# Kernel tuning notes

Hardware: AMD Instinct MI355X
Metric: run time of the kernel (lower is better)

Reference implementation:

```python
import jax, jax.numpy as jnp
import numpy as np

KSIZE = 3
PAD = (KSIZE - 1) // 2
SIG = 0.3 * ((KSIZE - 1) * 0.5 - 1) + 0.8  # sigma_space == sigma_density == 0.8
INV2S2 = 1.0 / (2.0 * SIG * SIG)


def _gauss_space():
    c = KSIZE // 2
    xs = np.arange(KSIZE, dtype=np.float32)
    gx, gy = np.meshgrid(xs, xs, indexing='xy')
    w = np.exp(-(((gx - c) ** 2 + (gy - c) ** 2)) * INV2S2)
    w = w / w.sum()
    return jnp.asarray(w, dtype=jnp.float32)


def _patches(x):
    # x: [N,C,H,W] -> [N,C,H,W,k,k], zero padding (matches F.pad value=0)
    H, W = x.shape[-2], x.shape[-1]
    xp = jnp.pad(x, ((0, 0), (0, 0), (PAD, PAD), (PAD, PAD)))
    rows = []
    for i in range(KSIZE):
        cols = [xp[:, :, i:i + H, j:j + W] for j in range(KSIZE)]
        rows.append(jnp.stack(cols, axis=-1))
    return jnp.stack(rows, axis=-2)


def setup_inputs() -> dict:
    key = jax.random.key(0)
    k1, k2, k3 = jax.random.split(key, 3)
    B, V, C, H, W = 2, 4, 3, 512, 512
    depth = jax.random.uniform(k1, (B, V, 1, H, W), dtype=jnp.float32)
    color = jax.random.uniform(k2, (B, V, C, H, W), dtype=jnp.float32)
    mask = jax.random.uniform(k3, (B, V, 1, H, W), dtype=jnp.float32)
    return {"depth": depth, "color": color, "mask": mask}


def reference(depth, color, mask):
    B, V, C, H, W = color.shape
    d = depth.reshape(B * V, 1, H, W)
    m = mask.reshape(B * V, 1, H, W)
    c = color.reshape(B * V, C, H, W)

    dp = _patches(d)  # [N,1,H,W,k,k]
    cp = _patches(c)  # [N,C,H,W,k,k]
    mp = _patches(m)  # [N,1,H,W,k,k]

    # depth (density) gaussian weight, normalized per-pixel over the window
    wd = jnp.exp(-((dp - d[..., None, None]) ** 2) * INV2S2)
    wd = wd / wd.sum(axis=(-1, -2), keepdims=True)

    # color gaussian weight summed over channels, normalized per-pixel
    wc = jnp.exp(-((cp - c[..., None, None]) ** 2) * INV2S2).sum(axis=1, keepdims=True)
    wc = wc / wc.sum(axis=(-1, -2), keepdims=True)

    ws = _gauss_space().reshape(1, 1, 1, 1, KSIZE, KSIZE)

    w = wd * wc * ws * mp + 1e-7  # [N,1,H,W,k,k]
    out = (w * cp).sum(axis=(-1, -2)) / w.sum(axis=(-1, -2))  # [N,C,H,W]
    return out.reshape(B, V, C, H, W)
```

## Files before the change

### kernel.cpp

```cpp
#include <hip/hip_runtime.h>


constexpr int HH = 512;
constexpr int WW = 512;
constexpr int HW = HH * WW;

#define KEXP (-1.1271055f)
#define E2(x) __builtin_amdgcn_exp2f(x)
#define WS0f 0.2724967f
#define WS1f 0.1247577f
#define WS2f 0.0571180f

__global__ __launch_bounds__(256) void bilateral_v6(
    const float* __restrict__ depth,
    const float* __restrict__ color,
    const float* __restrict__ mask,
    float* __restrict__ out)
{
    const int lane = threadIdx.x & 63;
    const int b    = blockIdx.x;
    const int logical = (b & 7) * 128 + (b >> 3);
    const int wg   = logical * 4 + (int)(threadIdx.x >> 6);
    const int n    = wg >> 9;
    const int rem  = wg & 511;
    const int hp   = rem >> 1;
    const int half = rem & 1;
    const int rA   = hp * 2;
    const int c0   = half * 256 + lane * 4;

    const float* dptr = depth + (size_t)n * HW;
    const float* mptr = mask  + (size_t)n * HW;
    const float* xptr = color + (size_t)n * 3 * HW;
    const float* yptr = xptr + HW;
    const float* zptr = xptr + 2 * HW;

    const bool hasL = (c0 > 0);
    const bool hasR = (c0 < WW - 4);

    float AD[6], AM[6], AX[6], AY[6], AZ[6];
    float BD[6], BM[6], BX[6], BY[6], BZ[6];
    float PD[6], PM[6], PX[6], PY[6], PZ[6];

#define LOADP(W, base, ro) do {                                              \
    const float4 _q = *reinterpret_cast<const float4*>((base) + (ro));       \
    W[1] = _q.x; W[2] = _q.y; W[3] = _q.z; W[4] = _q.w;                      \
    W[0] = hasL ? (base)[(ro) - 1] : 0.0f;                                   \
    W[5] = hasR ? (base)[(ro) + 4] : 0.0f;                                   \
} while (0)

#define LOADW(D_, M_, X_, Y_, Z_, r) do {                                    \
    const int _ro = (r) * WW + c0;                                           \
    LOADP(D_, dptr, _ro); LOADP(M_, mptr, _ro);                              \
    LOADP(X_, xptr, _ro); LOADP(Y_, yptr, _ro); LOADP(Z_, zptr, _ro);        \
} while (0)

    float aSwd[4], aSwc[4], aSt[4], aS0[4], aS1[4], aS2[4];
    float bSwd[4], bSwc[4], bSt[4], bS0[4], bS1[4], bS2[4];
    #pragma unroll
    for (int i = 0; i < 4; ++i) {
        aSwd[i]=0.f; aSwc[i]=0.f; aSt[i]=0.f; aS0[i]=0.f; aS1[i]=0.f; aS2[i]=0.f;
        bSwd[i]=0.f; bSwc[i]=0.f; bSt[i]=0.f; bS0[i]=0.f; bS1[i]=0.f; bS2[i]=0.f;
    }

#define HPASS(D_, M_, X_, Y_, Z_, Swd, Swc, St, S0, S1, S2) do {             \
    float hwd[5], hwc[5];                                                    \
    _Pragma("unroll") for (int j = 0; j < 5; ++j) {                          \
        const float dd = D_[j] - D_[j + 1];                                  \
        hwd[j] = E2(KEXP * dd * dd);                                         \
        const float f0 = X_[j] - X_[j + 1];                                  \
        const float f1 = Y_[j] - Y_[j + 1];                                  \
        const float f2 = Z_[j] - Z_[j + 1];                                  \
        hwc[j] = E2(KEXP * f0 * f0) + E2(KEXP * f1 * f1)                     \
               + E2(KEXP * f2 * f2);                                         \
    }                                                                        \
    _Pragma("unroll") for (int i = 0; i < 4; ++i) {                          \
        const int ci = i + 1;                                                \
        { const float t = (3.0f * WS0f) * M_[ci];      \
          Swd[i] += 1.0f; Swc[i] += 3.0f; St[i] += t;                        \
          S0[i] += t * X_[ci]; S1[i] += t * Y_[ci]; S2[i] += t * Z_[ci]; }   \
        { const float t = hwd[i] * hwc[i] * WS1f * M_[i];          \
          Swd[i] += hwd[i]; Swc[i] += hwc[i]; St[i] += t;                    \
          S0[i] += t * X_[i]; S1[i] += t * Y_[i]; S2[i] += t * Z_[i]; }      \
        { const float t = hwd[i+1] * hwc[i+1] * WS1f * M_[i+2];    \
          Swd[i] += hwd[i+1]; Swc[i] += hwc[i+1]; St[i] += t;                \
          S0[i] += t * X_[i+2]; S1[i] += t * Y_[i+2]; S2[i] += t * Z_[i+2];} \
    }                                                                        \
} while (0)

#define SIDE(TD, TM, TX, TY, TZ, RD, RX, RY, RZ, Swd, Swc, St, S0, S1, S2) do { \
    _Pragma("unroll") for (int i = 0; i < 4; ++i) {                          \
        const float cd = RD[i + 1];                                          \
        const float cx = RX[i + 1];                                          \
        const float cy = RY[i + 1];                                          \
        const float cz = RZ[i + 1];                                          \
        _Pragma("unroll") for (int dj = 0; dj < 3; ++dj) {                   \
            const int c = i + dj;                                            \
            const float dd = TD[c] - cd;                                     \
            const float wd = E2(KEXP * dd * dd);                             \
            const float f0 = TX[c] - cx;                                     \
            const float f1 = TY[c] - cy;                                     \
            const float f2 = TZ[c] - cz;                                     \
            const float wc = E2(KEXP * f0 * f0) + E2(KEXP * f1 * f1)         \
                           + E2(KEXP * f2 * f2);                             \
            const float ws = (dj == 1) ? WS1f : WS2f;                        \
            const float t = wd * wc * ws * TM[c];                            \
            Swd[i] += wd; Swc[i] += wc; St[i] += t;                          \
            S0[i] += t * TX[c]; S1[i] += t * TY[c]; S2[i] += t * TZ[c];      \
        }                                                                    \
    }                                                                        \
} while (0)

    const bool hasUp = (hp > 0);
    const bool hasDn = (hp < 255);

    LOADW(AD, AM, AX, AY, AZ, rA);
    LOADW(BD, BM, BX, BY, BZ, rA + 1);
    if (hasUp) LOADW(PD, PM, PX, PY, PZ, rA - 1);

    HPASS(AD, AM, AX, AY, AZ, aSwd, aSwc, aSt, aS0, aS1, aS2);
    HPASS(BD, BM, BX, BY, BZ, bSwd, bSwc, bSt, bS0, bS1, bS2);

    if (hasUp) {
        SIDE(PD, PM, PX, PY, PZ, AD, AX, AY, AZ,
             aSwd, aSwc, aSt, aS0, aS1, aS2);
    }

    if (hasDn) LOADW(PD, PM, PX, PY, PZ, rA + 2);

    #pragma unroll
    for (int a = 0; a < 6; ++a) {
        #pragma unroll
        for (int db = -1; db <= 1; ++db) {
            const int bb = a + db;
            if (bb < 0 || bb > 5) continue;
            const bool useA = (a >= 1 && a <= 4);
            const bool useB = (bb >= 1 && bb <= 4);
            if (!useA && !useB) continue;
            const float dd = AD[a] - BD[bb];
            const float pwd = E2(KEXP * dd * dd);
            const float f0 = AX[a] - BX[bb];
            const float f1 = AY[a] - BY[bb];
            const float f2 = AZ[a] - BZ[bb];
            const float pwc = E2(KEXP * f0 * f0) + E2(KEXP * f1 * f1)
                            + E2(KEXP * f2 * f2);
            const float g = pwd * pwc;
            const float ws = (db == 0) ? WS1f : WS2f;
            if (useA) {
                const int i = a - 1;
                const float t = g * ws * BM[bb];
                aSwd[i] += pwd; aSwc[i] += pwc; aSt[i] += t;
                aS0[i] += t * BX[bb]; aS1[i] += t * BY[bb]; aS2[i] += t * BZ[bb];
            }
            if (useB) {
                const int i = bb - 1;
                const float t = g * ws * AM[a];
                bSwd[i] += pwd; bSwc[i] += pwc; bSt[i] += t;
                bS0[i] += t * AX[a]; bS1[i] += t * AY[a]; bS2[i] += t * AZ[a];
            }
        }
    }

    if (hasDn) {
        SIDE(PD, PM, PX, PY, PZ, BD, BX, BY, BZ,
             bSwd, bSwc, bSt, bS0, bS1, bS2);
    }

    float oa0[4], oa1[4], oa2[4], ob0[4], ob1[4], ob2[4];
    #pragma unroll
    for (int i = 0; i < 4; ++i) {
        const float invA = __builtin_amdgcn_rcpf(aSt[i] + 9e-7f * aSwd[i] * aSwc[i]);
        oa0[i] = aS0[i] * invA; oa1[i] = aS1[i] * invA; oa2[i] = aS2[i] * invA;
        const float invB = __builtin_amdgcn_rcpf(bSt[i] + 9e-7f * bSwd[i] * bSwc[i]);
        ob0[i] = bS0[i] * invB; ob1[i] = bS1[i] * invB; ob2[i] = bS2[i] * invB;
    }

    float* po = out + (size_t)n * 3 * HW + rA * WW + c0;
    *reinterpret_cast<float4*>(po)               = make_float4(oa0[0], oa0[1], oa0[2], oa0[3]);
    *reinterpret_cast<float4*>(po + HW)          = make_float4(oa1[0], oa1[1], oa1[2], oa1[3]);
    *reinterpret_cast<float4*>(po + 2 * HW)      = make_float4(oa2[0], oa2[1], oa2[2], oa2[3]);
    *reinterpret_cast<float4*>(po + WW)          = make_float4(ob0[0], ob0[1], ob0[2], ob0[3]);
    *reinterpret_cast<float4*>(po + WW + HW)     = make_float4(ob1[0], ob1[1], ob1[2], ob1[3]);
    *reinterpret_cast<float4*>(po + WW + 2 * HW) = make_float4(ob2[0], ob2[1], ob2[2], ob2[3]);
}

extern "C" void kernel_launch(void* const* d_in, const int* in_sizes, int n_in,
                              void* d_out, int out_size, void* d_ws, size_t ws_size,
                              hipStream_t stream) {
    const float* depth = (const float*)d_in[0];
    const float* color = (const float*)d_in[1];
    const float* mask  = (const float*)d_in[2];
    float* out = (float*)d_out;

    bilateral_v6<<<1024, 256, 0, stream>>>(depth, color, mask, out);
}
```

Measured before the change: 27.36 us.

## Use aligned float2 halo loads, add occupancy hint, drop block swizzle, reorder loads

Halo columns are now fetched as aligned float2 loads (selecting one element) in place of scalar unaligned loads. The block-index XCD swizzle is removed, and __launch_bounds__ gains a min-blocks hint of 4. The below-row load is moved after the center computation to shorten register live ranges, and the HPASS accumulators are initialized by direct assignment. Together these aim to cut load instruction overhead and register pressure to raise occupancy, but they may lose L2 locality from the swizzle and reduce latency hiding for the late load.

```diff
diff --git a/kernel.cpp b/kernel.cpp
--- a/kernel.cpp
+++ b/kernel.cpp
@@ -1,9 +1,7 @@
 #include <hip/hip_runtime.h>
 
 
-constexpr int HH = 512;
-constexpr int WW = 512;
-constexpr int HW = HH * WW;
+constexpr int HH = 512, WW = 512, HW = HH * WW;
 
 #define KEXP (-1.1271055f)
 #define E2(x) __builtin_amdgcn_exp2f(x)
@@ -11,16 +9,14 @@
 #define WS1f 0.1247577f
 #define WS2f 0.0571180f
 
-__global__ __launch_bounds__(256) void bilateral_v6(
+__global__ __launch_bounds__(256, 4) void bilateral_v8(
     const float* __restrict__ depth,
     const float* __restrict__ color,
     const float* __restrict__ mask,
     float* __restrict__ out)
 {
     const int lane = threadIdx.x & 63;
-    const int b    = blockIdx.x;
-    const int logical = (b & 7) * 128 + (b >> 3);
-    const int wg   = logical * 4 + (int)(threadIdx.x >> 6);
+    const int wg   = blockIdx.x * 4 + (threadIdx.x >> 6);
     const int n    = wg >> 9;
     const int rem  = wg & 511;
     const int hp   = rem >> 1;
@@ -36,31 +32,30 @@
 
     const bool hasL = (c0 > 0);
     const bool hasR = (c0 < WW - 4);
+    const int  colL = hasL ? c0 - 2 : c0;
+    const int  colR = hasR ? c0 + 4 : c0;
 
+    float TD[6], TM[6], TX[6], TY[6], TZ[6];
     float AD[6], AM[6], AX[6], AY[6], AZ[6];
     float BD[6], BM[6], BX[6], BY[6], BZ[6];
-    float PD[6], PM[6], PX[6], PY[6], PZ[6];
 
-#define LOADP(W, base, ro) do {                                              \
-    const float4 _q = *reinterpret_cast<const float4*>((base) + (ro));       \
-    W[1] = _q.x; W[2] = _q.y; W[3] = _q.z; W[4] = _q.w;                      \
-    W[0] = hasL ? (base)[(ro) - 1] : 0.0f;                                   \
-    W[5] = hasR ? (base)[(ro) + 4] : 0.0f;                                   \
+#define LOADP(W, base, off) do {                                             \
+    const float4 _m = *reinterpret_cast<const float4*>((base) + (off) + c0); \
+    const float2 _l = *reinterpret_cast<const float2*>((base) + (off) + colL); \
+    const float2 _r = *reinterpret_cast<const float2*>((base) + (off) + colR); \
+    W[1] = _m.x; W[2] = _m.y; W[3] = _m.z; W[4] = _m.w;                      \
+    W[0] = hasL ? _l.y : 0.0f;                                               \
+    W[5] = hasR ? _r.x : 0.0f;                                               \
 } while (0)
 
 #define LOADW(D_, M_, X_, Y_, Z_, r) do {                                    \
-    const int _ro = (r) * WW + c0;                                           \
-    LOADP(D_, dptr, _ro); LOADP(M_, mptr, _ro);                              \
-    LOADP(X_, xptr, _ro); LOADP(Y_, yptr, _ro); LOADP(Z_, zptr, _ro);        \
+    const int _off = (r) * WW;                                               \
+    LOADP(D_, dptr, _off); LOADP(M_, mptr, _off);                            \
+    LOADP(X_, xptr, _off); LOADP(Y_, yptr, _off); LOADP(Z_, zptr, _off);     \
 } while (0)
 
     float aSwd[4], aSwc[4], aSt[4], aS0[4], aS1[4], aS2[4];
     float bSwd[4], bSwc[4], bSt[4], bS0[4], bS1[4], bS2[4];
-    #pragma unroll
-    for (int i = 0; i < 4; ++i) {
-        aSwd[i]=0.f; aSwc[i]=0.f; aSt[i]=0.f; aS0[i]=0.f; aS1[i]=0.f; aS2[i]=0.f;
-        bSwd[i]=0.f; bSwc[i]=0.f; bSt[i]=0.f; bS0[i]=0.f; bS1[i]=0.f; bS2[i]=0.f;
-    }
 
 #define HPASS(D_, M_, X_, Y_, Z_, Swd, Swc, St, S0, S1, S2) do {             \
     float hwd[5], hwc[5];                                                    \
@@ -75,19 +70,19 @@
     }                                                                        \
     _Pragma("unroll") for (int i = 0; i < 4; ++i) {                          \
         const int ci = i + 1;                                                \
-        { const float t = (3.0f * WS0f) * M_[ci];      \
-          Swd[i] += 1.0f; Swc[i] += 3.0f; St[i] += t;                        \
-          S0[i] += t * X_[ci]; S1[i] += t * Y_[ci]; S2[i] += t * Z_[ci]; }   \
-        { const float t = hwd[i] * hwc[i] * WS1f * M_[i];          \
-          Swd[i] += hwd[i]; Swc[i] += hwc[i]; St[i] += t;                    \
-          S0[i] += t * X_[i]; S1[i] += t * Y_[i]; S2[i] += t * Z_[i]; }      \
-        { const float t = hwd[i+1] * hwc[i+1] * WS1f * M_[i+2];    \
-          Swd[i] += hwd[i+1]; Swc[i] += hwc[i+1]; St[i] += t;                \
-          S0[i] += t * X_[i+2]; S1[i] += t * Y_[i+2]; S2[i] += t * Z_[i+2];} \
+        const float tc = (3.0f * WS0f) * M_[ci];                             \
+        const float tw = hwd[i]   * hwc[i]   * WS1f * M_[i];                 \
+        const float te = hwd[i+1] * hwc[i+1] * WS1f * M_[i+2];               \
+        Swd[i] = 1.0f + hwd[i] + hwd[i+1];                                   \
+        Swc[i] = 3.0f + hwc[i] + hwc[i+1];                                   \
+        St[i]  = tc + tw + te;                                               \
+        S0[i]  = tc * X_[ci] + tw * X_[i] + te * X_[i+2];                    \
+        S1[i]  = tc * Y_[ci] + tw * Y_[i] + te * Y_[i+2];                    \
+        S2[i]  = tc * Z_[ci] + tw * Z_[i] + te * Z_[i+2];                    \
     }                                                                        \
 } while (0)
 
-#define SIDE(TD, TM, TX, TY, TZ, RD, RX, RY, RZ, Swd, Swc, St, S0, S1, S2) do { \
+#define SIDE(D_, M_, X_, Y_, Z_, RD, RX, RY, RZ, Swd, Swc, St, S0, S1, S2) do { \
     _Pragma("unroll") for (int i = 0; i < 4; ++i) {                          \
         const float cd = RD[i + 1];                                          \
         const float cx = RX[i + 1];                                          \
@@ -95,17 +90,17 @@
         const float cz = RZ[i + 1];                                          \
         _Pragma("unroll") for (int dj = 0; dj < 3; ++dj) {                   \
             const int c = i + dj;                                            \
-            const float dd = TD[c] - cd;                                     \
+            const float dd = D_[c] - cd;                                     \
             const float wd = E2(KEXP * dd * dd);                             \
-            const float f0 = TX[c] - cx;                                     \
-            const float f1 = TY[c] - cy;                                     \
-            const float f2 = TZ[c] - cz;                                     \
+            const float f0 = X_[c] - cx;                                     \
+            const float f1 = Y_[c] - cy;                                     \
+            const float f2 = Z_[c] - cz;                                     \
             const float wc = E2(KEXP * f0 * f0) + E2(KEXP * f1 * f1)         \
                            + E2(KEXP * f2 * f2);                             \
             const float ws = (dj == 1) ? WS1f : WS2f;                        \
-            const float t = wd * wc * ws * TM[c];                            \
+            const float t = wd * wc * ws * M_[c];                            \
             Swd[i] += wd; Swc[i] += wc; St[i] += t;                          \
-            S0[i] += t * TX[c]; S1[i] += t * TY[c]; S2[i] += t * TZ[c];      \
+            S0[i] += t * X_[c]; S1[i] += t * Y_[c]; S2[i] += t * Z_[c];      \
         }                                                                    \
     }                                                                        \
 } while (0)
@@ -113,19 +108,15 @@
     const bool hasUp = (hp > 0);
     const bool hasDn = (hp < 255);
 
+    if (hasUp) LOADW(TD, TM, TX, TY, TZ, rA - 1);
     LOADW(AD, AM, AX, AY, AZ, rA);
     LOADW(BD, BM, BX, BY, BZ, rA + 1);
-    if (hasUp) LOADW(PD, PM, PX, PY, PZ, rA - 1);
 
     HPASS(AD, AM, AX, AY, AZ, aSwd, aSwc, aSt, aS0, aS1, aS2);
+    if (hasUp)
+        SIDE(TD, TM, TX, TY, TZ, AD, AX, AY, AZ,
+             aSwd, aSwc, aSt, aS0, aS1, aS2);
     HPASS(BD, BM, BX, BY, BZ, bSwd, bSwc, bSt, bS0, bS1, bS2);
-
-    if (hasUp) {
-        SIDE(PD, PM, PX, PY, PZ, AD, AX, AY, AZ,
-             aSwd, aSwc, aSt, aS0, aS1, aS2);
-    }
-
-    if (hasDn) LOADW(PD, PM, PX, PY, PZ, rA + 2);
 
     #pragma unroll
     for (int a = 0; a < 6; ++a) {
@@ -161,7 +152,8 @@
     }
 
     if (hasDn) {
-        SIDE(PD, PM, PX, PY, PZ, BD, BX, BY, BZ,
+        LOADW(TD, TM, TX, TY, TZ, rA + 2);
+        SIDE(TD, TM, TX, TY, TZ, BD, BX, BY, BZ,
              bSwd, bSwc, bSt, bS0, bS1, bS2);
     }
 
@@ -191,5 +183,5 @@
     const float* mask  = (const float*)d_in[2];
     float* out = (float*)d_out;
 
-    bilateral_v6<<<1024, 256, 0, stream>>>(depth, color, mask, out);
+    bilateral_v8<<<1024, 256, 0, stream>>>(depth, color, mask, out);
 }
```

Result: slower. 84.33 us (+208.2%).
